# Kernel tuning notes

Hardware: AMD Instinct MI355X
Metric: run time of the kernel (lower is better)

The kernel has to match this reference:

```python
import jax, jax.numpy as jnp
import numpy as np

EPS = 1e-6

def _aggregate(acc, right, a, w_acc, w_new):
    """Graded-logic weighted power mean aggregator.
    Andness a is mapped to a power-mean exponent r (a=0.5 -> r=1 arithmetic mean,
    a->1 -> r->-inf conjunctive, a->0 -> r->+inf disjunctive). Near r=0 the
    weighted geometric mean is the correct limit.
    """
    a_c = jnp.clip(a, EPS, 1.0 - EPS)
    r = (1.0 - 2.0 * a_c) / (a_c * (1.0 - a_c))
    use_geo = jnp.abs(r) < 1e-3
    r_safe = jnp.where(use_geo, 1.0, r)  # avoid inf in untaken branch
    acc_c = jnp.clip(acc, EPS, 1.0)
    right_c = jnp.clip(right, EPS, 1.0)
    pm = (w_acc * acc_c ** r_safe + w_new * right_c ** r_safe) ** (1.0 / r_safe)
    geo = acc_c ** w_acc * right_c ** w_new
    return jnp.where(use_geo, geo, pm)


def _forward(x, a_raw, w_raw):
    # andness mapping: sigmoid(a_raw) * 3 - 1  (normalize_andness=True)
    a_vec = jax.nn.sigmoid(a_raw) * 3.0 - 1.0
    # weight mapping: trainable + minmax normalization
    w_min, w_max = jnp.min(w_raw), jnp.max(w_raw)
    denom = jnp.maximum(w_max - w_min, 1e-8)
    w_new = jnp.clip((w_raw - w_min) / denom, 0.0, 1.0)
    w_acc = 1.0 - w_new

    leaf = x  # frozen identity permutation (is_frozen=True path)
    # first step (no NaN replacement in original)
    acc = _aggregate(leaf[:, 0], leaf[:, 1], a_vec[0], w_acc[0], w_new[0])

    def step(carry, inp):
        right, a_i, wa_i, wn_i = inp
        z = _aggregate(carry, right, a_i, wa_i, wn_i)
        z = jnp.where(jnp.isnan(z), a_i, z)  # per-step NaN patching
        return z, None

    xs = (leaf[:, 2:].T, a_vec[1:], w_acc[1:], w_new[1:])  # (L-1, B), (L-1,)...
    acc, _ = jax.lax.scan(step, acc, xs)
    return acc[:, None]  # (B, 1)


def setup_inputs() -> dict:
    key = jax.random.key(0)
    k1, k2 = jax.random.split(key)
    B, N = 524288, 64
    L = N - 1
    x = jax.random.uniform(k1, (B, N), dtype=jnp.float32)
    a_raw = jnp.zeros((L,), dtype=jnp.float32)
    w_raw = jax.random.uniform(k2, (L,), dtype=jnp.float32)
    return {"x": x, "a_raw": a_raw, "w_raw": w_raw}


def reference(x, a_raw, w_raw):
    return _forward(x, a_raw, w_raw)
```

## Files before the change

### kernel.cpp

```cpp
#include <hip/hip_runtime.h>

#define EPS 1e-6f
#define NSTEP 63

__device__ __forceinline__ float flog2(float x) { return __builtin_amdgcn_logf(x); }
__device__ __forceinline__ float fexp2(float x) { return __builtin_amdgcn_exp2f(x); }

__global__ __launch_bounds__(256, 4)
void vln_kernel(const float* __restrict__ x,
                const float* __restrict__ a_raw,
                const float* __restrict__ w_raw,
                float* __restrict__ out, int B) {
    __shared__ float s_wn[64];
    __shared__ float s_av[64];
    __shared__ float s_r[64];
    __shared__ int   s_geo[64];
    __shared__ int   s_allgeo;

    const int tid = threadIdx.x;

    if (tid < 64) {
        const int li = (tid < NSTEP) ? tid : 0;
        float w = w_raw[li];
        float wmin = w, wmax = w;
        #pragma unroll
        for (int off = 32; off > 0; off >>= 1) {
            wmin = fminf(wmin, __shfl_down(wmin, off));
            wmax = fmaxf(wmax, __shfl_down(wmax, off));
        }
        wmin = __shfl(wmin, 0);
        wmax = __shfl(wmax, 0);
        const float denom = fmaxf(wmax - wmin, 1e-8f);
        float wn = fminf(fmaxf((w - wmin) / denom, 0.0f), 1.0f);
        float ea = fexp2(-a_raw[li] * 1.4426950408889634f);
        float av = 3.0f / (1.0f + ea) - 1.0f;
        float ac = fminf(fmaxf(av, EPS), 1.0f - EPS);
        float r  = (1.0f - 2.0f * ac) / (ac * (1.0f - ac));
        int geo  = (fabsf(r) < 0.001f) ? 1 : 0;
        s_wn[tid] = wn;
        s_av[tid] = av;
        s_r[tid]  = r;
        s_geo[tid] = geo;
        unsigned long long m = __ballot(geo != 0 || tid >= NSTEP);
        if (tid == 0) s_allgeo = (m == ~0ULL) ? 1 : 0;
    }
    __syncthreads();

    const long long row = (long long)blockIdx.x * 256 + tid;
    if (row >= B) return;

    const float4* xr = (const float4*)(x + (size_t)row * 64);

    float4 nb0 = xr[0], nb1 = xr[1], nb2 = xr[2], nb3 = xr[3];

    const int allgeo = s_allgeo;

    if (allgeo) {
        float Lacc = 0.0f;
        #pragma unroll
        for (int c = 0; c < 4; ++c) {
            float f[16];
            ((float4*)f)[0] = nb0; ((float4*)f)[1] = nb1;
            ((float4*)f)[2] = nb2; ((float4*)f)[3] = nb3;
            if (c < 3) {
                nb0 = xr[4*c+4]; nb1 = xr[4*c+5];
                nb2 = xr[4*c+6]; nb3 = xr[4*c+7];
            }
            float l[16];
            #pragma unroll
            for (int k = 0; k < 16; ++k)
                l[k] = flog2(fminf(fmaxf(f[k], EPS), 1.0f));
            #pragma unroll
            for (int k = 0; k < 16; ++k) {
                const int g = 16*c + k;
                if (g == 0) { Lacc = l[0]; continue; }
                const float wn = s_wn[g - 1];
                Lacc = fmaf(wn, l[k] - Lacc, Lacc);
            }
        }
        out[row] = fexp2(Lacc);
    } else {
        float Lacc = 0.0f;
        float lin  = 0.0f;
        int use_lin = 0;
        #pragma unroll
        for (int c = 0; c < 4; ++c) {
            float f[16];
            ((float4*)f)[0] = nb0; ((float4*)f)[1] = nb1;
            ((float4*)f)[2] = nb2; ((float4*)f)[3] = nb3;
            if (c < 3) {
                nb0 = xr[4*c+4]; nb1 = xr[4*c+5];
                nb2 = xr[4*c+6]; nb3 = xr[4*c+7];
            }
            float l[16];
            #pragma unroll
            for (int k = 0; k < 16; ++k)
                l[k] = flog2(fminf(fmaxf(f[k], EPS), 1.0f));
            #pragma unroll
            for (int k = 0; k < 16; ++k) {
                const int g = 16*c + k;
                if (g == 0) { Lacc = l[0]; continue; }
                const int i = g - 1;
                const float wn = s_wn[i];
                const float lr = l[k];
                if (s_geo[i]) {
                    Lacc = fmaf(wn, lr - Lacc, Lacc);
                    use_lin = 0;
                } else {
                    const float r = s_r[i];
                    const float pa = fexp2(r * Lacc);
                    const float pb = fexp2(r * lr);
                    const float s  = (1.0f - wn) * pa + wn * pb;
                    float z = fexp2(flog2(s) / r);
                    if (i > 0 && (z != z)) z = s_av[i];
                    lin = z; use_lin = 1;
                    Lacc = flog2(fminf(fmaxf(z, EPS), 1.0f));
                }
            }
        }
        out[row] = use_lin ? lin : fexp2(Lacc);
    }
}

extern "C" void kernel_launch(void* const* d_in, const int* in_sizes, int n_in,
                              void* d_out, int out_size, void* d_ws, size_t ws_size,
                              hipStream_t stream) {
    const float* x     = (const float*)d_in[0];
    const float* a_raw = (const float*)d_in[1];
    const float* w_raw = (const float*)d_in[2];
    float* out = (float*)d_out;
    const int B = out_size;
    const int blocks = (B + 255) / 256;
    vln_kernel<<<blocks, 256, 0, stream>>>(x, a_raw, w_raw, out, B);
}
```

Before: 198.9 us.

## Stage row tiles through swizzled LDS for coalesced global loads

```diff
diff --git a/kernel.cpp b/kernel.cpp
--- a/kernel.cpp
+++ b/kernel.cpp
@@ -6,11 +6,12 @@
 __device__ __forceinline__ float flog2(float x) { return __builtin_amdgcn_logf(x); }
 __device__ __forceinline__ float fexp2(float x) { return __builtin_amdgcn_exp2f(x); }
 
-__global__ __launch_bounds__(256, 4)
+__global__ __launch_bounds__(256, 2)
 void vln_kernel(const float* __restrict__ x,
                 const float* __restrict__ a_raw,
                 const float* __restrict__ w_raw,
                 float* __restrict__ out, int B) {
+    __shared__ float4 tile[4][1024];
     __shared__ float s_wn[64];
     __shared__ float s_av[64];
     __shared__ float s_r[64];
@@ -46,36 +47,49 @@
     }
     __syncthreads();
 
-    const long long row = (long long)blockIdx.x * 256 + tid;
-    if (row >= B) return;
+    const int wave = tid >> 6;
+    const int lane = tid & 63;
+    const long long rowbase = (long long)blockIdx.x * 256 + wave * 64;
+    const long long row = rowbase + lane;
 
-    const float4* xr = (const float4*)(x + (size_t)row * 64);
+    float4 f[16];
 
-    float4 nb0 = xr[0], nb1 = xr[1], nb2 = xr[2], nb3 = xr[3];
+    if (rowbase + 64 <= (long long)B) {
+        const float4* g = (const float4*)(x + (size_t)rowbase * 64);
+        float4* tl = tile[wave];
+        #pragma unroll
+        for (int t = 0; t < 16; ++t) {
+            float4 v = g[t * 64 + lane];
+            const int r  = t * 4 + (lane >> 4);
+            const int gi = lane & 15;
+            tl[r * 16 + (gi ^ (r & 15))] = v;
+        }
+        #pragma unroll
+        for (int q = 0; q < 16; ++q)
+            f[q] = tl[lane * 16 + (q ^ (lane & 15))];
+    } else if (row < (long long)B) {
+        const float4* xr = (const float4*)(x + (size_t)row * 64);
+        #pragma unroll
+        for (int q = 0; q < 16; ++q) f[q] = xr[q];
+    }
 
-    const int allgeo = s_allgeo;
+    if (row >= (long long)B) return;
 
-    if (allgeo) {
+    if (s_allgeo) {
         float Lacc = 0.0f;
         #pragma unroll
-        for (int c = 0; c < 4; ++c) {
-            float f[16];
-            ((float4*)f)[0] = nb0; ((float4*)f)[1] = nb1;
-            ((float4*)f)[2] = nb2; ((float4*)f)[3] = nb3;
-            if (c < 3) {
-                nb0 = xr[4*c+4]; nb1 = xr[4*c+5];
-                nb2 = xr[4*c+6]; nb3 = xr[4*c+7];
-            }
-            float l[16];
+        for (int q = 0; q < 16; ++q) {
+            float el[4];
+            el[0] = flog2(fminf(fmaxf(f[q].x, EPS), 1.0f));
+            el[1] = flog2(fminf(fmaxf(f[q].y, EPS), 1.0f));
+            el[2] = flog2(fminf(fmaxf(f[q].z, EPS), 1.0f));
+            el[3] = flog2(fminf(fmaxf(f[q].w, EPS), 1.0f));
             #pragma unroll
-            for (int k = 0; k < 16; ++k)
-                l[k] = flog2(fminf(fmaxf(f[k], EPS), 1.0f));
-            #pragma unroll
-            for (int k = 0; k < 16; ++k) {
-                const int g = 16*c + k;
-                if (g == 0) { Lacc = l[0]; continue; }
-                const float wn = s_wn[g - 1];
-                Lacc = fmaf(wn, l[k] - Lacc, Lacc);
+            for (int j = 0; j < 4; ++j) {
+                const int gidx = 4 * q + j;
+                if (gidx == 0) { Lacc = el[0]; continue; }
+                const float wn = s_wn[gidx - 1];
+                Lacc = fmaf(wn, el[j] - Lacc, Lacc);
             }
         }
         out[row] = fexp2(Lacc);
@@ -84,30 +98,24 @@
         float lin  = 0.0f;
         int use_lin = 0;
         #pragma unroll
-        for (int c = 0; c < 4; ++c) {
-            float f[16];
-            ((float4*)f)[0] = nb0; ((float4*)f)[1] = nb1;
-            ((float4*)f)[2] = nb2; ((float4*)f)[3] = nb3;
-            if (c < 3) {
-                nb0 = xr[4*c+4]; nb1 = xr[4*c+5];
-                nb2 = xr[4*c+6]; nb3 = xr[4*c+7];
-            }
-            float l[16];
+        for (int q = 0; q < 16; ++q) {
+            float el[4];
+            el[0] = flog2(fminf(fmaxf(f[q].x, EPS), 1.0f));
+            el[1] = flog2(fminf(fmaxf(f[q].y, EPS), 1.0f));
+            el[2] = flog2(fminf(fmaxf(f[q].z, EPS), 1.0f));
+            el[3] = flog2(fminf(fmaxf(f[q].w, EPS), 1.0f));
             #pragma unroll
-            for (int k = 0; k < 16; ++k)
-                l[k] = flog2(fminf(fmaxf(f[k], EPS), 1.0f));
-            #pragma unroll
-            for (int k = 0; k < 16; ++k) {
-                const int g = 16*c + k;
-                if (g == 0) { Lacc = l[0]; continue; }
-                const int i = g - 1;
+            for (int j = 0; j < 4; ++j) {
+                const int gidx = 4 * q + j;
+                if (gidx == 0) { Lacc = el[0]; continue; }
+                const int i = gidx - 1;
                 const float wn = s_wn[i];
-                const float lr = l[k];
+                const float lr = el[j];
                 if (s_geo[i]) {
                     Lacc = fmaf(wn, lr - Lacc, Lacc);
                     use_lin = 0;
                 } else {
-                    const float r = s_r[i];
+                    const float r  = s_r[i];
                     const float pa = fexp2(r * Lacc);
                     const float pb = fexp2(r * lr);
                     const float s  = (1.0f - wn) * pa + wn * pb;
```

Result: faster. 193.1 us (-2.9%).
